# Kernel optimization log

Hardware: AMD Instinct MI355X
Metric: run time of the kernel (lower is better)

The kernel has to match this reference:

```python
import jax, jax.numpy as jnp
import numpy as np

HIST_LEN = 100  # STDP history cap in the original module


def setup_inputs() -> dict:
    key = jax.random.key(0)
    ks = jax.random.split(key, 5)
    H, B = 1024, 16384
    return {
        "x": jax.random.normal(ks[0], (B, H), dtype=jnp.float32),
        "weights": jax.random.normal(ks[1], (H, H), dtype=jnp.float32) * 0.1,
        "meta_plasticity": jnp.ones((H,), dtype=jnp.float32),
        "pre_hist": jax.random.normal(ks[2], (HIST_LEN, H), dtype=jnp.float32) * 0.1,
        "post_hist": jax.random.normal(ks[3], (HIST_LEN, H), dtype=jnp.float32) * 0.1,
        "activity_history": jnp.zeros((1000,), dtype=jnp.float32),
        "history_pointer": 5,
        "stdp_window": jnp.float32(20.0),
        "stdp_decay": jnp.float32(0.1),
        "target_activity": jnp.float32(0.1),
        "homeostatic_rate": jnp.float32(0.01),
        "meta_learning_rate": jnp.float32(0.001),
    }


def reference(x, weights, meta_plasticity, pre_hist, post_hist,
              activity_history, history_pointer, stdp_window, stdp_decay,
              target_activity, homeostatic_rate, meta_learning_rate):
    # --- forward matmul: weights * meta_plasticity scales columns (broadcast over rows)
    output = x @ (weights * meta_plasticity)  # [B, H]

    # --- STDP update (vectorized form of the python loop over the history) ---
    # append current mean activities, pop oldest (steady-state length == HIST_LEN)
    pre = jnp.concatenate([pre_hist[1:], x.mean(axis=0)[None]], axis=0)       # [L, H]
    post = jnp.concatenate([post_hist[1:], output.mean(axis=0)[None]], axis=0)
    L = HIST_LEN
    i = jnp.arange(L, dtype=jnp.float32)
    dt = (L - i) * stdp_window
    w = 0.01 * jnp.exp(-dt * stdp_decay)                                      # [L]
    pos_w = jnp.where(i < L - 1, w, 0.0)   # i < len-1 branch
    neg_w = jnp.where(i > 0, w, 0.0)       # i > 0 branch
    # sum_i pos_w[i] * outer(post[-1], pre[i]) = outer(post[-1], pos_w @ pre)
    dW = jnp.outer(post[-1], pos_w @ pre) - jnp.outer(neg_w @ post, pre[-1])
    new_w = jnp.clip(weights + dW, -1.0, 1.0)

    # --- homeostatic plasticity ---
    hist = activity_history.at[history_pointer].set(output.mean())
    activity_diff = target_activity - hist.mean()
    new_w = jnp.clip(new_w * (1.0 + homeostatic_rate * activity_diff), -1.0, 1.0)

    # --- meta plasticity ---
    new_meta = jnp.clip(
        meta_plasticity + meta_learning_rate * (output.mean(axis=0) - meta_plasticity),
        0.0, 2.0)

    return output, new_w, new_meta, hist
```

## Files before the change

kernel.cpp:

```cpp
#include <hip/hip_runtime.h>
#include <hip/hip_bf16.h>

#define H 1024
#define BATCH 16384

typedef unsigned short u16;
typedef u16 u16x8 __attribute__((ext_vector_type(8)));
typedef __bf16 bf16x8 __attribute__((ext_vector_type(8)));
typedef float f32x4 __attribute__((ext_vector_type(4)));

typedef __attribute__((address_space(3))) unsigned int lds_uint;
typedef __attribute__((address_space(1))) const unsigned int glob_uint;

__device__ __forceinline__ u16 f2bf(float f) {
  unsigned int u = __float_as_uint(f);
  u += 0x7fffu + ((u >> 16) & 1u);
  return (u16)(u >> 16);
}

#define WS_XSUMP   0
#define WS_XSUM    (WS_XSUMP + 256 * H)
#define WS_ORAWP   (WS_XSUM + H)
#define WS_POSVP   (WS_ORAWP + 16 * H)
#define WS_NEGHP   (WS_POSVP + 5 * H)
#define WS_SCRATCH (WS_NEGHP + 5 * H)
#define WS_BF16    (WS_SCRATCH + 16)

__global__ __launch_bounds__(256) void prep_kernel(const float* __restrict__ X,
                                                   const float* __restrict__ W,
                                                   u16* __restrict__ Xb,
                                                   u16* __restrict__ Wbt,
                                                   float* __restrict__ ws,
                                                   const float* __restrict__ pre,
                                                   const float* __restrict__ post,
                                                   const float* __restrict__ win,
                                                   const float* __restrict__ dec) {
  __shared__ __align__(16) u16 t[64][72];
  const int b = blockIdx.x, tid = threadIdx.x;
  if (b < 256) {
    size_t r0 = (size_t)b * 64;
    float s0 = 0.f, s1 = 0.f, s2 = 0.f, s3 = 0.f;
#pragma unroll 4
    for (int r = 0; r < 64; ++r) {
      size_t off = (r0 + r) * H + tid * 4;
      const float4 v = *(const float4*)&X[off];
      ushort4 h;
      h.x = f2bf(v.x); h.y = f2bf(v.y); h.z = f2bf(v.z); h.w = f2bf(v.w);
      *(ushort4*)&Xb[off] = h;
      s0 += v.x; s1 += v.y; s2 += v.z; s3 += v.w;
    }
    float* row = &ws[WS_XSUMP + b * H];
    row[tid * 4 + 0] = s0; row[tid * 4 + 1] = s1;
    row[tid * 4 + 2] = s2; row[tid * 4 + 3] = s3;
  } else if (b < 512) {
    const int b2 = b - 256;
    const int n0 = (b2 & 15) * 64, k0 = (b2 >> 4) * 64;
    const int rb = tid >> 4, c4 = tid & 15;
#pragma unroll
    for (int i = 0; i < 4; ++i) {
      int r = rb + i * 16;
      const float4 v = *(const float4*)&W[(size_t)(k0 + r) * H + n0 + c4 * 4];
      t[c4 * 4 + 0][r] = f2bf(v.x);
      t[c4 * 4 + 1][r] = f2bf(v.y);
      t[c4 * 4 + 2][r] = f2bf(v.z);
      t[c4 * 4 + 3][r] = f2bf(v.w);
    }
    __syncthreads();
    const int seg = tid & 7;
#pragma unroll
    for (int p = 0; p < 2; ++p) {
      int wr = p * 32 + (tid >> 3);
      *(u16x8*)&Wbt[(size_t)(n0 + wr) * H + k0 + seg * 8] = *(const u16x8*)&t[wr][seg * 8];
    }
  } else {
    const int b2 = b - 512;
    const int col = (b2 & 3) * 256 + tid;
    const int seg = b2 >> 2;
    const int t0 = 1 + seg * 20;
    int tend = t0 + 20; if (tend > 100) tend = 100;
    float wd = win[0] * dec[0];
    float ps = 0.f, ns = 0.f;
    for (int tt = t0; tt < tend; ++tt) {
      float w = 0.01f * expf(-(float)(101 - tt) * wd);
      ps += w * pre[tt * H + col];
      if (tt >= 2) ns += w * post[tt * H + col];
    }
    ws[WS_POSVP + seg * H + col] = ps;
    ws[WS_NEGHP + seg * H + col] = ns;
  }
}

__global__ __launch_bounds__(512, 2) void gemm_vm_kernel(const u16* __restrict__ Xb,
                                                         const u16* __restrict__ Wbt,
                                                         const float* __restrict__ meta,
                                                         const float* __restrict__ W,
                                                         float* __restrict__ ws,
                                                         float* __restrict__ out) {
  __shared__ __align__(16) u16 lds[65536];

  const int b = blockIdx.x, tid = threadIdx.x;

  const int tile = ((b & 7) << 5) | (b >> 3);
  const int mt = tile >> 2, nt = tile & 3;
  const size_t row0 = (size_t)mt * 256;
  const int col0 = nt * 256;
  const int wid = tid >> 6, lane = tid & 63;
  const int wm = wid >> 2, wn = wid & 3;
  const int quad = lane >> 4, l16 = lane & 15;
  const int xsw = l16 & 7;

  const int srow = lane >> 3;
  const int schunk = (lane & 7) ^ (srow & 7);

  auto stageA = [&](int t, int h) {
#pragma unroll
    for (int s = 0; s < 2; ++s) {
      const u16* ga = &Xb[(row0 + h * 128 + s * 64 + wid * 8 + srow) * H + t * 64 + schunk * 8];
      lds_uint* ld = (lds_uint*)&lds[(((2 * t + h) & 3) * 8192) + s * 4096 + wid * 512];
      __builtin_amdgcn_global_load_lds((glob_uint*)ga, ld, 16, 0, 0);
    }
  };
  auto stageB = [&](int t, int h) {
#pragma unroll
    for (int s = 0; s < 2; ++s) {
      const u16* gb = &Wbt[(size_t)(col0 + h * 128 + s * 64 + wid * 8 + srow) * H + t * 64 + schunk * 8];
      lds_uint* ld = (lds_uint*)&lds[32768 + (((2 * t + h) & 3) * 8192) + s * 4096 + wid * 512];
      __builtin_amdgcn_global_load_lds((glob_uint*)gb, ld, 16, 0, 0);
    }
  };

  f32x4 acc[8][4];
#pragma unroll
  for (int i = 0; i < 8; ++i)
#pragma unroll
    for (int j = 0; j < 4; ++j) acc[i][j] = (f32x4){0.f, 0.f, 0.f, 0.f};

  stageA(0, 0); stageA(0, 1); stageB(0, 0); stageB(0, 1); stageB(1, 0); stageB(1, 1);
  asm volatile("s_waitcnt vmcnt(4)" ::: "memory");
  __builtin_amdgcn_s_barrier();

  for (int it = 0; it < 8; ++it) {
    const bool last = (it == 7);
#pragma unroll
    for (int hf = 0; hf < 2; ++hf) {
      const int tc = 2 * it + hf;
      const int aslot = ((2 * tc + wm) & 3) * 8192;
      const int bslot = 32768 + ((2 * tc + (wn >> 1)) & 3) * 8192;
      const int brl = (wn & 1) * 64;
      bf16x8 bv[4][2];
#pragma unroll
      for (int sub = 0; sub < 4; ++sub) {
        if (hf == 0) {
          if (sub == 0)      stageA(2 * it + 1, 0);
          else if (sub == 1) stageA(2 * it + 1, 1);
          else if (sub == 2) { if (!last) stageB(2 * it + 2, 0); }
          else               { if (!last) stageB(2 * it + 2, 1); }
        } else {
          if (sub == 0)      { if (!last) stageA(2 * it + 2, 0); }
          else if (sub == 1) { if (!last) stageA(2 * it + 2, 1); }
          else if (sub == 2) { if (!last) stageB(2 * it + 3, 0); }
          else               { if (!last) stageB(2 * it + 3, 1); }
        }
        if (sub == 0) {
#pragma unroll
          for (int fn = 0; fn < 4; ++fn)
#pragma unroll
            for (int ks = 0; ks < 2; ++ks)
              bv[fn][ks] = __builtin_bit_cast(bf16x8,
                *(const u16x8*)&lds[bslot + (brl + fn * 16 + l16) * 64 + (((ks * 4 + quad) ^ xsw) * 8)]);
        }
        bf16x8 av[2][2];
#pragma unroll
        for (int fi = 0; fi < 2; ++fi)
#pragma unroll
          for (int ks = 0; ks < 2; ++ks)
            av[fi][ks] = __builtin_bit_cast(bf16x8,
              *(const u16x8*)&lds[aslot + ((sub * 2 + fi) * 16 + l16) * 64 + (((ks * 4 + quad) ^ xsw) * 8)]);

        __builtin_amdgcn_s_barrier();
        asm volatile("s_waitcnt lgkmcnt(0)" ::: "memory");
        __builtin_amdgcn_sched_barrier(0);
        __builtin_amdgcn_s_setprio(1);
#pragma unroll
        for (int fi = 0; fi < 2; ++fi)
#pragma unroll
          for (int fn = 0; fn < 4; ++fn)
#pragma unroll
            for (int ks = 0; ks < 2; ++ks)
              acc[sub * 2 + fi][fn] = __builtin_amdgcn_mfma_f32_16x16x32_bf16(
                  av[fi][ks], bv[fn][ks], acc[sub * 2 + fi][fn], 0, 0, 0);
        __builtin_amdgcn_s_setprio(0);
        if (sub == 3) {
          if (hf == 0 && last) asm volatile("s_waitcnt vmcnt(0)" ::: "memory");
          else                 asm volatile("s_waitcnt vmcnt(4)" ::: "memory");
        }
        __builtin_amdgcn_s_barrier();
      }
    }
  }

  float mcol[4];
#pragma unroll
  for (int fn = 0; fn < 4; ++fn) mcol[fn] = meta[col0 + wn * 64 + fn * 16 + l16];
#pragma unroll
  for (int fm = 0; fm < 8; ++fm) {
#pragma unroll
    for (int fn = 0; fn < 4; ++fn) {
      const int col = col0 + wn * 64 + fn * 16 + l16;
#pragma unroll
      for (int r = 0; r < 4; ++r) {
        size_t row = row0 + wm * 128 + fm * 16 + quad * 4 + r;
        out[row * H + col] = acc[fm][fn][r] * mcol[fn];
      }
    }
  }

  if (b < 64) {
    __syncthreads();
    float* xs = (float*)lds;
    const int jx = b & 3, ky = b >> 2;
    if (tid < 64) {
      float s = 0.f;
      const float* p = &ws[WS_XSUMP + ky * 64 + tid];
#pragma unroll 8
      for (int q = 0; q < 256; ++q) s += p[q * H];
      xs[tid] = s;
      if (jx == 0) ws[WS_XSUM + ky * 64 + tid] = s;
    }
    __syncthreads();
    if (tid < 256) {
      const int j = jx * 256 + tid;
      float s = 0.f;
#pragma unroll 8
      for (int k = 0; k < 64; ++k) s += xs[k] * W[(size_t)(ky * 64 + k) * H + j];
      ws[WS_ORAWP + ky * H + j] = s * (1.0f / (float)BATCH);
    }
  }
}

__global__ __launch_bounds__(256) void tail_kernel(const float* __restrict__ W,
                                                   const float* __restrict__ meta,
                                                   const float* __restrict__ act,
                                                   const int* __restrict__ ptr,
                                                   const float* __restrict__ targ,
                                                   const float* __restrict__ homeo,
                                                   const float* __restrict__ mlr,
                                                   const float* __restrict__ win,
                                                   const float* __restrict__ dec,
                                                   const float* __restrict__ ws,
                                                   float* __restrict__ out_w,
                                                   float* __restrict__ meta_out,
                                                   float* __restrict__ hist_out) {
  __shared__ float r1[4], r2[4];
  const int r = blockIdx.x;
  const int t = threadIdx.x;
  const int c4 = t * 4;

  f32x4 oraw = (f32x4){0.f, 0.f, 0.f, 0.f};
#pragma unroll
  for (int i = 0; i < 16; ++i) {
    const float4 v = *(const float4*)&ws[WS_ORAWP + i * H + c4];
    oraw[0] += v.x; oraw[1] += v.y; oraw[2] += v.z; oraw[3] += v.w;
  }
  const float4 mv = *(const float4*)&meta[c4];
  f32x4 om;
  om[0] = mv.x * oraw[0]; om[1] = mv.y * oraw[1];
  om[2] = mv.z * oraw[2]; om[3] = mv.w * oraw[3];

  float s1 = om[0] + om[1] + om[2] + om[3];
  float s2 = 0.f;
#pragma unroll
  for (int j = 0; j < 4; ++j) {
    int idx = t + j * 256;
    if (idx < 1000) s2 += act[idx];
  }
#pragma unroll
  for (int o = 32; o > 0; o >>= 1) {
    s1 += __shfl_down(s1, o, 64);
    s2 += __shfl_down(s2, o, 64);
  }
  if ((t & 63) == 0) { r1[t >> 6] = s1; r2[t >> 6] = s2; }
  __syncthreads();
  const float ts1 = r1[0] + r1[1] + r1[2] + r1[3];
  const float ts2 = r2[0] + r2[1] + r2[2] + r2[3];
  const float total_mean = ts1 / (float)H;
  const int p = ptr[0];
  const float hist_mean = (ts2 - act[p] + total_mean) / 1000.f;
  const float scale = 1.f + homeo[0] * (targ[0] - hist_mean);
  const float w99 = 0.01f * expf(-win[0] * dec[0]);

  float oraw_r = 0.f;
#pragma unroll
  for (int i = 0; i < 16; ++i) oraw_r += ws[WS_ORAWP + i * H + r];
  const float om_r = meta[r] * oraw_r;
  float negh_r = 0.f;
#pragma unroll
  for (int i = 0; i < 5; ++i) negh_r += ws[WS_NEGHP + i * H + r];
  const float neg_r = negh_r + w99 * om_r;

  f32x4 pv = (f32x4){0.f, 0.f, 0.f, 0.f};
#pragma unroll
  for (int i = 0; i < 5; ++i) {
    const float4 v = *(const float4*)&ws[WS_POSVP + i * H + c4];
    pv[0] += v.x; pv[1] += v.y; pv[2] += v.z; pv[3] += v.w;
  }
  const float4 xv = *(const float4*)&ws[WS_XSUM + c4];
  float xx[4] = {xv.x, xv.y, xv.z, xv.w};
  const float4 wv = *(const float4*)&W[(size_t)r * H + c4];
  float wx[4] = {wv.x, wv.y, wv.z, wv.w};
  float4 o;
  float ox[4];
#pragma unroll
  for (int i = 0; i < 4; ++i) {
    float v = wx[i] + om_r * pv[i] - neg_r * (xx[i] * (1.0f / (float)BATCH));
    v = fminf(fmaxf(v, -1.f), 1.f);
    v = v * scale;
    ox[i] = fminf(fmaxf(v, -1.f), 1.f);
  }
  o.x = ox[0]; o.y = ox[1]; o.z = ox[2]; o.w = ox[3];
  *(float4*)&out_w[(size_t)r * H + c4] = o;

  if (r == 0) {
    float4 nm;
    float nx[4] = {mv.x, mv.y, mv.z, mv.w};
    float nr[4];
#pragma unroll
    for (int i = 0; i < 4; ++i) {
      float v = nx[i] + mlr[0] * (om[i] - nx[i]);
      nr[i] = fminf(fmaxf(v, 0.f), 2.f);
    }
    nm.x = nr[0]; nm.y = nr[1]; nm.z = nr[2]; nm.w = nr[3];
    *(float4*)&meta_out[c4] = nm;
#pragma unroll
    for (int j = 0; j < 4; ++j) {
      int idx = t + j * 256;
      if (idx < 1000) hist_out[idx] = (idx == p) ? total_mean : act[idx];
    }
  }
}

__global__ __launch_bounds__(256) void colsum_kernel(const float* __restrict__ x,
                                                     float* __restrict__ xsum) {
  int col = blockIdx.x * 256 + threadIdx.x;
  size_t r0 = (size_t)blockIdx.y * 256;
  float s = 0.f;
#pragma unroll 8
  for (int r = 0; r < 256; ++r) s += x[(r0 + r) * H + col];
  atomicAdd(&xsum[col], s);
}

__global__ __launch_bounds__(256) void gemm_fallback_kernel(const float* __restrict__ X,
                                                            const float* __restrict__ W,
                                                            const float* __restrict__ meta,
                                                            float* __restrict__ out) {
  __shared__ __align__(16) u16 lA[128][40];
  __shared__ __align__(16) u16 lB[128][40];
  const int tid = threadIdx.x;
  const int wave = tid >> 6;
  const int lane = tid & 63;
  const int quad = lane >> 4;
  const int l16 = lane & 15;
  const int wm = wave >> 1, wn = wave & 1;
  const size_t row0 = (size_t)blockIdx.x * 128;
  const int col0 = blockIdx.y * 128;
  f32x4 acc[4][4];
#pragma unroll
  for (int i = 0; i < 4; ++i)
#pragma unroll
    for (int j = 0; j < 4; ++j) acc[i][j] = (f32x4){0.f, 0.f, 0.f, 0.f};
  for (int k0 = 0; k0 < H; k0 += 32) {
#pragma unroll
    for (int i = 0; i < 4; ++i) {
      int idx = i * 256 + tid;
      int r = idx >> 3, c4 = idx & 7;
      const float4 v = *(const float4*)&X[(row0 + r) * H + k0 + c4 * 4];
      ushort4 h;
      h.x = f2bf(v.x); h.y = f2bf(v.y); h.z = f2bf(v.z); h.w = f2bf(v.w);
      *(ushort4*)&lA[r][c4 * 4] = h;
    }
#pragma unroll
    for (int i = 0; i < 4; ++i) {
      int idx = i * 256 + tid;
      int kk = idx >> 5, c4 = idx & 31;
      const float4 v = *(const float4*)&W[(size_t)(k0 + kk) * H + col0 + c4 * 4];
      lB[c4 * 4 + 0][kk] = f2bf(v.x);
      lB[c4 * 4 + 1][kk] = f2bf(v.y);
      lB[c4 * 4 + 2][kk] = f2bf(v.z);
      lB[c4 * 4 + 3][kk] = f2bf(v.w);
    }
    __syncthreads();
    bf16x8 av[4], bv[4];
#pragma unroll
    for (int f = 0; f < 4; ++f) {
      av[f] = __builtin_bit_cast(bf16x8, *(const u16x8*)&lA[wm * 64 + f * 16 + l16][quad * 8]);
      bv[f] = __builtin_bit_cast(bf16x8, *(const u16x8*)&lB[wn * 64 + f * 16 + l16][quad * 8]);
    }
#pragma unroll
    for (int fm = 0; fm < 4; ++fm)
#pragma unroll
      for (int fn = 0; fn < 4; ++fn)
        acc[fm][fn] = __builtin_amdgcn_mfma_f32_16x16x32_bf16(av[fm], bv[fn], acc[fm][fn], 0, 0, 0);
    __syncthreads();
  }
  float mcol[4];
#pragma unroll
  for (int fn = 0; fn < 4; ++fn) mcol[fn] = meta[col0 + wn * 64 + fn * 16 + l16];
#pragma unroll
  for (int fm = 0; fm < 4; ++fm) {
#pragma unroll
    for (int fn = 0; fn < 4; ++fn) {
      int col = col0 + wn * 64 + fn * 16 + l16;
#pragma unroll
      for (int r = 0; r < 4; ++r) {
        size_t row = row0 + wm * 64 + fm * 16 + quad * 4 + r;
        out[row * H + col] = acc[fm][fn][r] * mcol[fn];
      }
    }
  }
}

__global__ __launch_bounds__(256) void vecmat_kernel(const float* __restrict__ W,
                                                     const float* __restrict__ xsum,
                                                     float* __restrict__ outraw) {
  int j = blockIdx.x * 256 + threadIdx.x;
  int k0 = blockIdx.y * 64;
  float s = 0.f;
#pragma unroll 8
  for (int k = 0; k < 64; ++k) s += xsum[k0 + k] * W[(size_t)(k0 + k) * H + j];
  atomicAdd(&outraw[j], s * (1.0f / (float)BATCH));
}

__global__ __launch_bounds__(256) void stdpvec_kernel(const float* __restrict__ pre,
                                                      const float* __restrict__ post,
                                                      const float* __restrict__ win,
                                                      const float* __restrict__ dec,
                                                      float* __restrict__ posv,
                                                      float* __restrict__ negh) {
  int col = blockIdx.x * 256 + threadIdx.x;
  int t0 = 1 + blockIdx.y * 20;
  float wd = win[0] * dec[0];
  float ps = 0.f, ns = 0.f;
  int tend = t0 + 20;
  if (tend > 100) tend = 100;
  for (int t = t0; t < tend; ++t) {
    float w = 0.01f * expf(-(float)(101 - t) * wd);
    ps += w * pre[t * H + col];
    if (t >= 2) ns += w * post[t * H + col];
  }
  atomicAdd(&posv[col], ps);
  atomicAdd(&negh[col], ns);
}

__global__ __launch_bounds__(1024) void finalize_kernel(const float* __restrict__ meta,
                                                        const float* __restrict__ act,
                                                        const int* __restrict__ ptr,
                                                        const float* __restrict__ targ,
                                                        const float* __restrict__ homeo,
                                                        const float* __restrict__ mlr,
                                                        const float* __restrict__ outraw,
                                                        float* __restrict__ outmean,
                                                        float* __restrict__ scalep,
                                                        float* __restrict__ meta_out,
                                                        float* __restrict__ hist_out) {
  __shared__ float r1[16], r2[16];
  __shared__ float sc[2];
  int t = threadIdx.x;
  float om = meta[t] * outraw[t];
  outmean[t] = om;
  float a = (t < 1000) ? act[t] : 0.f;
  float s1 = om, s2 = a;
#pragma unroll
  for (int o = 32; o > 0; o >>= 1) {
    s1 += __shfl_down(s1, o, 64);
    s2 += __shfl_down(s2, o, 64);
  }
  if ((t & 63) == 0) { r1[t >> 6] = s1; r2[t >> 6] = s2; }
  __syncthreads();
  if (t == 0) {
    float ts1 = 0.f, ts2 = 0.f;
#pragma unroll
    for (int i = 0; i < 16; ++i) { ts1 += r1[i]; ts2 += r2[i]; }
    float total_mean = ts1 / (float)H;
    int p = ptr[0];
    float hist_mean = (ts2 - act[p] + total_mean) / 1000.f;
    float diff = targ[0] - hist_mean;
    sc[0] = 1.f + homeo[0] * diff;
    sc[1] = total_mean;
    scalep[0] = sc[0];
  }
  __syncthreads();
  float nm = meta[t] + mlr[0] * (om - meta[t]);
  nm = fminf(fmaxf(nm, 0.f), 2.f);
  meta_out[t] = nm;
  if (t < 1000) hist_out[t] = (t == ptr[0]) ? sc[1] : act[t];
}

__global__ __launch_bounds__(256) void neww_kernel(const float* __restrict__ W,
                                                   const float* __restrict__ outmean,
                                                   const float* __restrict__ posv,
                                                   const float* __restrict__ negh,
                                                   const float* __restrict__ xsum,
                                                   const float* __restrict__ scalep,
                                                   const float* __restrict__ win,
                                                   const float* __restrict__ dec,
                                                   float* __restrict__ out) {
  int idx4 = blockIdx.x * 256 + threadIdx.x;
  int rr = idx4 >> 8;
  int c4 = (idx4 & 255) * 4;
  float w99 = 0.01f * expf(-win[0] * dec[0]);
  float scale = scalep[0];
  float om_r = outmean[rr];
  float neg_r = negh[rr] + w99 * om_r;
  const float4 wv = *(const float4*)&W[(size_t)rr * H + c4];
  const float4 pv = *(const float4*)&posv[c4];
  const float4 xv = *(const float4*)&xsum[c4];
  float4 o;
  float vx[4] = {wv.x, wv.y, wv.z, wv.w};
  float px[4] = {pv.x, pv.y, pv.z, pv.w};
  float xx[4] = {xv.x, xv.y, xv.z, xv.w};
  float ox[4];
#pragma unroll
  for (int i = 0; i < 4; ++i) {
    float v = vx[i] + om_r * px[i] - neg_r * (xx[i] * (1.0f / (float)BATCH));
    v = fminf(fmaxf(v, -1.f), 1.f);
    v = v * scale;
    ox[i] = fminf(fmaxf(v, -1.f), 1.f);
  }
  o.x = ox[0]; o.y = ox[1]; o.z = ox[2]; o.w = ox[3];
  *(float4*)&out[(size_t)rr * H + c4] = o;
}

extern "C" void kernel_launch(void* const* d_in, const int* in_sizes, int n_in,
                              void* d_out, int out_size, void* d_ws, size_t ws_size,
                              hipStream_t stream) {
  const float* x     = (const float*)d_in[0];
  const float* W     = (const float*)d_in[1];
  const float* meta  = (const float*)d_in[2];
  const float* pre   = (const float*)d_in[3];
  const float* post  = (const float*)d_in[4];
  const float* act   = (const float*)d_in[5];
  const int*   ptr   = (const int*)d_in[6];
  const float* win   = (const float*)d_in[7];
  const float* dec   = (const float*)d_in[8];
  const float* targ  = (const float*)d_in[9];
  const float* homeo = (const float*)d_in[10];
  const float* mlr   = (const float*)d_in[11];

  float* out_y    = (float*)d_out;
  float* out_w    = out_y + (size_t)BATCH * H;
  float* out_meta = out_w + (size_t)H * H;
  float* out_hist = out_meta + H;

  float* ws = (float*)d_ws;
  u16* Xb  = (u16*)(ws + WS_BF16);
  u16* Wbt = Xb + (size_t)BATCH * H;

  const size_t ws_need = (size_t)WS_BF16 * sizeof(float) +
                         ((size_t)BATCH * H + (size_t)H * H) * sizeof(u16);

  if (ws_size >= ws_need) {
    prep_kernel<<<532, 256, 0, stream>>>(x, W, Xb, Wbt, ws, pre, post, win, dec);
    gemm_vm_kernel<<<256, 512, 0, stream>>>(Xb, Wbt, meta, W, ws, out_y);
    tail_kernel<<<1024, 256, 0, stream>>>(W, meta, act, ptr, targ, homeo, mlr,
                                          win, dec, ws, out_w, out_meta, out_hist);
  } else {
    float* xsum    = ws;
    float* outraw  = ws + 1024;
    float* outmean = ws + 2048;
    float* posv    = ws + 3072;
    float* negh    = ws + 4096;
    float* scalep  = ws + 5120;
    hipMemsetAsync(d_ws, 0, 6144 * sizeof(float), stream);
    colsum_kernel<<<dim3(4, 64), 256, 0, stream>>>(x, xsum);
    gemm_fallback_kernel<<<dim3(128, 8), 256, 0, stream>>>(x, W, meta, out_y);
    vecmat_kernel<<<dim3(4, 16), 256, 0, stream>>>(W, xsum, outraw);
    stdpvec_kernel<<<dim3(4, 5), 256, 0, stream>>>(pre, post, win, dec, posv, negh);
    finalize_kernel<<<1, 1024, 0, stream>>>(meta, act, ptr, targ, homeo, mlr,
                                            outraw, outmean, scalep, out_meta, out_hist);
    neww_kernel<<<1024, 256, 0, stream>>>(W, outmean, posv, negh, xsum, scalep, win, dec, out_w);
  }
}
```

Before: 204.1 us.

## Restructure GEMM main loop to two barriers per K-tile and offload vecmat to extra blocks

The GEMM main loop drops from four barrier-separated sub-steps per half-tile to two larger phases per K-tile. Each phase loads four A fragments and issues 32 MFMAs, and A/B staging is interleaved between the phases, cutting barrier and waitcnt overhead. The x column-sum and vector-matrix product that tile blocks 0-63 ran after their epilogue now runs in 64 extra blocks appended to the grid, so the GEMM blocks no longer have a serial tail. The risks are higher register pressure from the larger av arrays and the need for the changed vmcnt accounting to keep the LDS slots hazard-free.

```diff
diff --git a/kernel.cpp b/kernel.cpp
--- a/kernel.cpp
+++ b/kernel.cpp
@@ -100,6 +100,29 @@
 
   const int b = blockIdx.x, tid = threadIdx.x;
 
+  if (b >= 256) {
+    float* xs = (float*)lds;
+    const int b2 = b - 256;
+    const int jx = b2 & 3, ky = b2 >> 2;
+    if (tid < 64) {
+      float s = 0.f;
+      const float* p = &ws[WS_XSUMP + ky * 64 + tid];
+#pragma unroll 8
+      for (int q = 0; q < 256; ++q) s += p[q * H];
+      xs[tid] = s;
+      if (jx == 0) ws[WS_XSUM + ky * 64 + tid] = s;
+    }
+    __syncthreads();
+    if (tid < 256) {
+      const int j = jx * 256 + tid;
+      float s = 0.f;
+#pragma unroll 8
+      for (int k = 0; k < 64; ++k) s += xs[k] * W[(size_t)(ky * 64 + k) * H + j];
+      ws[WS_ORAWP + ky * H + j] = s * (1.0f / (float)BATCH);
+    }
+    return;
+  }
+
   const int tile = ((b & 7) << 5) | (b >> 3);
   const int mt = tile >> 2, nt = tile & 3;
   const size_t row0 = (size_t)mt * 256;
@@ -136,67 +159,70 @@
     for (int j = 0; j < 4; ++j) acc[i][j] = (f32x4){0.f, 0.f, 0.f, 0.f};
 
   stageA(0, 0); stageA(0, 1); stageB(0, 0); stageB(0, 1); stageB(1, 0); stageB(1, 1);
-  asm volatile("s_waitcnt vmcnt(4)" ::: "memory");
+  asm volatile("s_waitcnt vmcnt(2)" ::: "memory");
   __builtin_amdgcn_s_barrier();
 
-  for (int it = 0; it < 8; ++it) {
-    const bool last = (it == 7);
-#pragma unroll
-    for (int hf = 0; hf < 2; ++hf) {
-      const int tc = 2 * it + hf;
-      const int aslot = ((2 * tc + wm) & 3) * 8192;
-      const int bslot = 32768 + ((2 * tc + (wn >> 1)) & 3) * 8192;
-      const int brl = (wn & 1) * 64;
-      bf16x8 bv[4][2];
-#pragma unroll
-      for (int sub = 0; sub < 4; ++sub) {
-        if (hf == 0) {
-          if (sub == 0)      stageA(2 * it + 1, 0);
-          else if (sub == 1) stageA(2 * it + 1, 1);
-          else if (sub == 2) { if (!last) stageB(2 * it + 2, 0); }
-          else               { if (!last) stageB(2 * it + 2, 1); }
-        } else {
-          if (sub == 0)      { if (!last) stageA(2 * it + 2, 0); }
-          else if (sub == 1) { if (!last) stageA(2 * it + 2, 1); }
-          else if (sub == 2) { if (!last) stageB(2 * it + 3, 0); }
-          else               { if (!last) stageB(2 * it + 3, 1); }
-        }
-        if (sub == 0) {
-#pragma unroll
-          for (int fn = 0; fn < 4; ++fn)
-#pragma unroll
-            for (int ks = 0; ks < 2; ++ks)
-              bv[fn][ks] = __builtin_bit_cast(bf16x8,
-                *(const u16x8*)&lds[bslot + (brl + fn * 16 + l16) * 64 + (((ks * 4 + quad) ^ xsw) * 8)]);
-        }
-        bf16x8 av[2][2];
-#pragma unroll
-        for (int fi = 0; fi < 2; ++fi)
+  for (int t = 0; t < 16; ++t) {
+    const int aslot = ((2 * t + wm) & 3) * 8192;
+    const int bslot = 32768 + ((2 * t + (wn >> 1)) & 3) * 8192;
+    const int brl = (wn & 1) * 64;
+    bf16x8 bv[4][2];
+
+    if (t < 15) { stageA(t + 1, 0); stageA(t + 1, 1); }
+#pragma unroll
+    for (int fn = 0; fn < 4; ++fn)
+#pragma unroll
+      for (int ks = 0; ks < 2; ++ks)
+        bv[fn][ks] = __builtin_bit_cast(bf16x8,
+          *(const u16x8*)&lds[bslot + (brl + fn * 16 + l16) * 64 + (((ks * 4 + quad) ^ xsw) * 8)]);
+    {
+      bf16x8 av[4][2];
+#pragma unroll
+      for (int fi = 0; fi < 4; ++fi)
+#pragma unroll
+        for (int ks = 0; ks < 2; ++ks)
+          av[fi][ks] = __builtin_bit_cast(bf16x8,
+            *(const u16x8*)&lds[aslot + (fi * 16 + l16) * 64 + (((ks * 4 + quad) ^ xsw) * 8)]);
+      asm volatile("s_waitcnt lgkmcnt(0)" ::: "memory");
+      __builtin_amdgcn_sched_barrier(0);
+      __builtin_amdgcn_s_setprio(1);
+#pragma unroll
+      for (int fi = 0; fi < 4; ++fi)
+#pragma unroll
+        for (int fn = 0; fn < 4; ++fn)
 #pragma unroll
           for (int ks = 0; ks < 2; ++ks)
-            av[fi][ks] = __builtin_bit_cast(bf16x8,
-              *(const u16x8*)&lds[aslot + ((sub * 2 + fi) * 16 + l16) * 64 + (((ks * 4 + quad) ^ xsw) * 8)]);
-
-        __builtin_amdgcn_s_barrier();
-        asm volatile("s_waitcnt lgkmcnt(0)" ::: "memory");
-        __builtin_amdgcn_sched_barrier(0);
-        __builtin_amdgcn_s_setprio(1);
-#pragma unroll
-        for (int fi = 0; fi < 2; ++fi)
-#pragma unroll
-          for (int fn = 0; fn < 4; ++fn)
-#pragma unroll
-            for (int ks = 0; ks < 2; ++ks)
-              acc[sub * 2 + fi][fn] = __builtin_amdgcn_mfma_f32_16x16x32_bf16(
-                  av[fi][ks], bv[fn][ks], acc[sub * 2 + fi][fn], 0, 0, 0);
-        __builtin_amdgcn_s_setprio(0);
-        if (sub == 3) {
-          if (hf == 0 && last) asm volatile("s_waitcnt vmcnt(0)" ::: "memory");
-          else                 asm volatile("s_waitcnt vmcnt(4)" ::: "memory");
-        }
-        __builtin_amdgcn_s_barrier();
-      }
-    }
+            acc[fi][fn] = __builtin_amdgcn_mfma_f32_16x16x32_bf16(
+                av[fi][ks], bv[fn][ks], acc[fi][fn], 0, 0, 0);
+      __builtin_amdgcn_s_setprio(0);
+    }
+    __builtin_amdgcn_s_barrier();
+
+    if (t < 14) { stageB(t + 2, 0); stageB(t + 2, 1); }
+    {
+      bf16x8 av[4][2];
+#pragma unroll
+      for (int fi = 0; fi < 4; ++fi)
+#pragma unroll
+        for (int ks = 0; ks < 2; ++ks)
+          av[fi][ks] = __builtin_bit_cast(bf16x8,
+            *(const u16x8*)&lds[aslot + ((4 + fi) * 16 + l16) * 64 + (((ks * 4 + quad) ^ xsw) * 8)]);
+      asm volatile("s_waitcnt lgkmcnt(0)" ::: "memory");
+      __builtin_amdgcn_sched_barrier(0);
+      __builtin_amdgcn_s_setprio(1);
+#pragma unroll
+      for (int fi = 0; fi < 4; ++fi)
+#pragma unroll
+        for (int fn = 0; fn < 4; ++fn)
+#pragma unroll
+          for (int ks = 0; ks < 2; ++ks)
+            acc[4 + fi][fn] = __builtin_amdgcn_mfma_f32_16x16x32_bf16(
+                av[fi][ks], bv[fn][ks], acc[4 + fi][fn], 0, 0, 0);
+      __builtin_amdgcn_s_setprio(0);
+    }
+    if (t < 14)       asm volatile("s_waitcnt vmcnt(2)" ::: "memory");
+    else if (t == 14) asm volatile("s_waitcnt vmcnt(0)" ::: "memory");
+    __builtin_amdgcn_s_barrier();
   }
 
   float mcol[4];
@@ -212,28 +238,6 @@
         size_t row = row0 + wm * 128 + fm * 16 + quad * 4 + r;
         out[row * H + col] = acc[fm][fn][r] * mcol[fn];
       }
-    }
-  }
-
-  if (b < 64) {
-    __syncthreads();
-    float* xs = (float*)lds;
-    const int jx = b & 3, ky = b >> 2;
-    if (tid < 64) {
-      float s = 0.f;
-      const float* p = &ws[WS_XSUMP + ky * 64 + tid];
-#pragma unroll 8
-      for (int q = 0; q < 256; ++q) s += p[q * H];
-      xs[tid] = s;
-      if (jx == 0) ws[WS_XSUM + ky * 64 + tid] = s;
-    }
-    __syncthreads();
-    if (tid < 256) {
-      const int j = jx * 256 + tid;
-      float s = 0.f;
-#pragma unroll 8
-      for (int k = 0; k < 64; ++k) s += xs[k] * W[(size_t)(ky * 64 + k) * H + j];
-      ws[WS_ORAWP + ky * H + j] = s * (1.0f / (float)BATCH);
     }
   }
 }
@@ -560,7 +564,7 @@
 
   if (ws_size >= ws_need) {
     prep_kernel<<<532, 256, 0, stream>>>(x, W, Xb, Wbt, ws, pre, post, win, dec);
-    gemm_vm_kernel<<<256, 512, 0, stream>>>(Xb, Wbt, meta, W, ws, out_y);
+    gemm_vm_kernel<<<320, 512, 0, stream>>>(Xb, Wbt, meta, W, ws, out_y);
     tail_kernel<<<1024, 256, 0, stream>>>(W, meta, act, ptr, targ, homeo, mlr,
                                           win, dec, ws, out_w, out_meta, out_hist);
   } else {
```

Result: no change. 203.7 us (-0.2%).
